# Optimization experiments

Hardware: AMD Instinct MI355X
Metric: run time of the kernel (lower is better)

Reference implementation:

```python
import jax, jax.numpy as jnp
import numpy as np

B, S, H = 64, 512, 768
A1, C1 = 100, 300          # token-attention and sentence-classifier hidden sizes
BETA = 1.0                 # soft_attention_beta
SLW, TLW, RLW = 1.0, 1.0, 0.01  # loss weights


def setup_inputs() -> dict:
    key = jax.random.key(0)
    ks = jax.random.split(key, 12)
    hidden_states = jax.random.normal(ks[0], (B, S, H), jnp.float32)
    # token_attention: Linear(H,100) -> Tanh -> Linear(100,1) -> Sigmoid
    w1 = jax.random.normal(ks[1], (H, A1), jnp.float32) * 0.02
    b1 = jnp.zeros((A1,), jnp.float32)
    w2 = jax.random.normal(ks[2], (A1, 1), jnp.float32) * 0.02
    b2 = jnp.zeros((1,), jnp.float32)
    # sentence_classification: Linear(H,300) -> Tanh -> Linear(300,1) -> Sigmoid
    sw1 = jax.random.normal(ks[3], (H, C1), jnp.float32) * 0.02
    sb1 = jnp.zeros((C1,), jnp.float32)
    sw2 = jax.random.normal(ks[4], (C1, 1), jnp.float32) * 0.02
    sb2 = jnp.zeros((1,), jnp.float32)
    offset_mapping = jax.random.randint(ks[5], (B, S, 2), 0, 4).astype(jnp.int32)
    offset_mapping = offset_mapping.at[:, 0, 0].set(0)  # first token starts a word
    # labels in {-1, 0, 1}; -1 = ignore
    labels = jax.random.randint(ks[6], (B, S), -1, 2).astype(jnp.float32)
    return {
        "hidden_states": hidden_states,
        "w1": w1, "b1": b1, "w2": w2, "b2": b2,
        "sw1": sw1, "sb1": sb1, "sw2": sw2, "sb2": sb2,
        "labels": labels,
        "offset_mapping": offset_mapping,
    }


def _forward(hidden_states, w1, b1, w2, b2, sw1, sb1, sw2, sb2, labels, offset_mapping):
    # token attention scores in (0,1): [B, S]
    token_att = jax.nn.sigmoid(
        jnp.tanh(hidden_states @ w1 + b1) @ w2 + b2
    )[..., 0]

    # ragged per-word subword max-pooling (segment-max along the sequence)
    not_subword = offset_mapping[:, :, 0] == 0                 # [B, S] word starts
    seg = jnp.maximum(jnp.cumsum(not_subword.astype(jnp.int32), axis=1) - 1, 0)

    def _seg_max(vals, seg_ids):
        return jax.ops.segment_max(vals, seg_ids, num_segments=S)

    segmax = jax.vmap(_seg_max)(token_att, seg)                # [B, S] per-word max
    word_att = jnp.where(not_subword, jnp.take_along_axis(segmax, seg, axis=1), 0.0)

    # mask: labeled tokens that are word starts
    token_mask = ((labels != -1) & not_subword).astype(token_att.dtype)
    masked = word_att * token_mask                              # token_logits [B, S]

    # beta-normalized soft attention pooling over hidden states
    p = masked ** BETA
    att_norm = p / jnp.sum(p, axis=1, keepdims=True)            # [B, S]
    pooled = jnp.einsum("bsh,bs->bh", hidden_states, att_norm)  # [B, H]

    sent = jax.nn.sigmoid(jnp.tanh(pooled @ sw1 + sb1) @ sw2 + sb2)  # [B, 1]

    # losses (MSE with reduction='sum')
    sentence_labels = jnp.max(labels, axis=1, keepdims=True)    # [B, 1]
    sentence_loss = jnp.sum((sent - sentence_labels) ** 2)
    zero_labels = jnp.where(labels != -1, labels, 0.0)
    token_loss = jnp.sum((masked - zero_labels) ** 2)
    ones_masked = jnp.where(masked == 0, 1.0, masked)
    reg_a = jnp.sum(jnp.min(ones_masked, axis=1, keepdims=True) ** 2)
    reg_b = jnp.sum((jnp.max(masked, axis=1, keepdims=True) - sentence_labels) ** 2)
    total = SLW * sentence_loss + TLW * token_loss + RLW * (reg_a + reg_b)
    return total, sentence_loss, token_loss, reg_a, reg_b, masked, sent


def reference(hidden_states, w1, b1, w2, b2, sw1, sb1, sw2, sb2, labels, offset_mapping):
    return _forward(hidden_states, w1, b1, w2, b2, sw1, sb1, sw2, sb2,
                    labels, offset_mapping)
```

## Files before the change

### kernel.cpp

```cpp
#include <hip/hip_runtime.h>
#include <math.h>

#define BB 64
#define SS 512
#define HH 768
#define AA1 100
#define CC1 300

typedef __bf16 bf16x8 __attribute__((ext_vector_type(8)));
typedef float f32x4 __attribute__((ext_vector_type(4)));

#ifndef __has_builtin
#define __has_builtin(x) 0
#endif
#if __has_builtin(__builtin_amdgcn_global_load_lds)
#define HAVE_GLL 1
#else
#define HAVE_GLL 0
#endif

#define AS1 __attribute__((address_space(1)))
#define AS3 __attribute__((address_space(3)))

__global__ __launch_bounds__(256) void k_prep(const float* __restrict__ w1,
                                              __bf16* __restrict__ w1i) {
    int idx = blockIdx.x * 256 + threadIdx.x;
    int j = idx % 112;
    int r = idx / 112;
    int e = r & 7, g = r >> 3;
    int k = (g >> 2) * 32 + (g & 3) * 8 + e;
    float v = (j < AA1) ? w1[k * AA1 + j] : 0.f;
    w1i[((size_t)g * 112 + j) * 8 + e] = (__bf16)v;
}

__global__ __launch_bounds__(256) void k_token_att(
        const float* __restrict__ hs, const __bf16* __restrict__ w1i,
        const float* __restrict__ b1, const float* __restrict__ w2,
        const float* __restrict__ b2, float* __restrict__ token_att) {
    __shared__ __attribute__((aligned(16))) float lA[4096];
    __shared__ __attribute__((aligned(16))) __bf16 lB[3584];

    const int tid = threadIdx.x;
    const int tok0 = blockIdx.x * 128;
    const int w = tid >> 6, lane = tid & 63;
    const int q = lane >> 4, ln = lane & 15;
    const int t0 = w * 32 + ln;
    const int t1 = t0 + 16;

    f32x4 acc0[7], acc1[7];
#pragma unroll
    for (int n = 0; n < 7; n++) {
        acc0[n] = (f32x4){0.f, 0.f, 0.f, 0.f};
        acc1[n] = (f32x4){0.f, 0.f, 0.f, 0.f};
    }

    const int p0 = (2 * q) ^ (ln & 7);
    const int p1 = (2 * q + 1) ^ (ln & 7);

    for (int kt = 0; kt < 24; kt++) {
        const int ko = kt * 32;
#pragma unroll
        for (int it = 0; it < 4; it++) {
            int i = tid + it * 256;
            int tt = i >> 3, c = (i & 7) ^ (tt & 7);
            const float* g = hs + (size_t)(tok0 + tt) * HH + ko + c * 4;
#if HAVE_GLL
            __builtin_amdgcn_global_load_lds((AS1 void*)g,
                    (AS3 void*)(lA + (it * 256 + w * 64) * 4), 16, 0, 0);
#else
            *(f32x4*)&lA[i * 4] = *(const f32x4*)g;
#endif
        }
        {
            const __bf16* gb0 = w1i + (size_t)kt * 3584 + (size_t)tid * 8;
#if HAVE_GLL
            __builtin_amdgcn_global_load_lds((AS1 void*)gb0,
                    (AS3 void*)(lB + (w * 64) * 8), 16, 0, 0);
            if (w < 3) {
                const __bf16* gb1 = w1i + (size_t)kt * 3584 + (size_t)(tid + 256) * 8;
                __builtin_amdgcn_global_load_lds((AS1 void*)gb1,
                        (AS3 void*)(lB + (256 + w * 64) * 8), 16, 0, 0);
            }
#else
            *(bf16x8*)&lB[(size_t)tid * 8] = *(const bf16x8*)gb0;
            if (tid < 192) {
                const __bf16* gb1 = w1i + (size_t)kt * 3584 + (size_t)(tid + 256) * 8;
                *(bf16x8*)&lB[(size_t)(tid + 256) * 8] = *(const bf16x8*)gb1;
            }
#endif
        }
        __syncthreads();
        f32x4 a00 = *(f32x4*)&lA[(t0 * 8 + p0) * 4];
        f32x4 a01 = *(f32x4*)&lA[(t0 * 8 + p1) * 4];
        f32x4 a10 = *(f32x4*)&lA[(t1 * 8 + p0) * 4];
        f32x4 a11 = *(f32x4*)&lA[(t1 * 8 + p1) * 4];
        bf16x8 af0, af1;
#pragma unroll
        for (int e = 0; e < 4; e++) {
            af0[e] = (__bf16)a00[e]; af0[e + 4] = (__bf16)a01[e];
            af1[e] = (__bf16)a10[e]; af1[e + 4] = (__bf16)a11[e];
        }
#pragma unroll
        for (int n = 0; n < 7; n++) {
            bf16x8 bf = *(bf16x8*)&lB[((size_t)q * 112 + n * 16 + ln) * 8];
            acc0[n] = __builtin_amdgcn_mfma_f32_16x16x32_bf16(af0, bf, acc0[n], 0, 0, 0);
            acc1[n] = __builtin_amdgcn_mfma_f32_16x16x32_bf16(af1, bf, acc1[n], 0, 0, 0);
        }
        __syncthreads();
    }

    float s0 = 0.f, s1 = 0.f, s2 = 0.f, s3 = 0.f;
    float u0 = 0.f, u1 = 0.f, u2 = 0.f, u3 = 0.f;
#pragma unroll
    for (int n = 0; n < 7; n++) {
        int j = n * 16 + ln;
        if (j < AA1) {
            float bj = b1[j], wj = w2[j];
            s0 += tanhf(acc0[n][0] + bj) * wj;
            s1 += tanhf(acc0[n][1] + bj) * wj;
            s2 += tanhf(acc0[n][2] + bj) * wj;
            s3 += tanhf(acc0[n][3] + bj) * wj;
            u0 += tanhf(acc1[n][0] + bj) * wj;
            u1 += tanhf(acc1[n][1] + bj) * wj;
            u2 += tanhf(acc1[n][2] + bj) * wj;
            u3 += tanhf(acc1[n][3] + bj) * wj;
        }
    }
#pragma unroll
    for (int off = 1; off < 16; off <<= 1) {
        s0 += __shfl_xor(s0, off); s1 += __shfl_xor(s1, off);
        s2 += __shfl_xor(s2, off); s3 += __shfl_xor(s3, off);
        u0 += __shfl_xor(u0, off); u1 += __shfl_xor(u1, off);
        u2 += __shfl_xor(u2, off); u3 += __shfl_xor(u3, off);
    }
    if (ln == 0) {
        float bb = b2[0];
        int base0 = tok0 + w * 32 + q * 4;
        int base1 = base0 + 16;
        token_att[base0 + 0] = 1.f / (1.f + expf(-(s0 + bb)));
        token_att[base0 + 1] = 1.f / (1.f + expf(-(s1 + bb)));
        token_att[base0 + 2] = 1.f / (1.f + expf(-(s2 + bb)));
        token_att[base0 + 3] = 1.f / (1.f + expf(-(s3 + bb)));
        token_att[base1 + 0] = 1.f / (1.f + expf(-(u0 + bb)));
        token_att[base1 + 1] = 1.f / (1.f + expf(-(u1 + bb)));
        token_att[base1 + 2] = 1.f / (1.f + expf(-(u2 + bb)));
        token_att[base1 + 3] = 1.f / (1.f + expf(-(u3 + bb)));
    }
}

__global__ __launch_bounds__(512) void k_mask(
        const float* __restrict__ token_att, const float* __restrict__ labels,
        const int* __restrict__ offm, float* __restrict__ masked_out,
        float* __restrict__ cw_g, short* __restrict__ cs_g,
        int* __restrict__ nnz_g, float* __restrict__ inv_g,
        float4* __restrict__ stats_g, float* __restrict__ out) {
    __shared__ int smax[512];
    __shared__ int wscan[8];
    __shared__ int wscan2[8];
    __shared__ float wred[5][8];

    const int b = blockIdx.x, s = threadIdx.x;
    const int lane = s & 63, wv = s >> 6;
    if (b == 0 && s < 5) out[s] = 0.f;
    const int ns = (offm[(b * SS + s) * 2] == 0) ? 1 : 0;

    int v = ns;
#pragma unroll
    for (int off = 1; off < 64; off <<= 1) {
        int o = __shfl_up(v, off);
        if (lane >= off) v += o;
    }
    if (lane == 63) wscan[wv] = v;
    smax[s] = 0;
    __syncthreads();
    int woff = 0;
    for (int i = 0; i < 8; i++) woff += (i < wv) ? wscan[i] : 0;
    const int seg = max(v + woff - 1, 0);

    const float ta = token_att[b * SS + s];
    atomicMax(&smax[seg], __float_as_int(ta));
    __syncthreads();

    const float wa = ns ? __int_as_float(smax[seg]) : 0.f;
    const float lab = labels[b * SS + s];
    const float m = (lab != -1.f && ns) ? wa : 0.f;
    masked_out[b * SS + s] = m;

    const float zl = (lab != -1.f) ? lab : 0.f;
    const float tl = (m - zl) * (m - zl);
    const float ones = (m == 0.f) ? 1.f : m;

    float r0 = m, r1 = tl, r2 = m, r3 = ones, r4 = lab;
#pragma unroll
    for (int off = 32; off > 0; off >>= 1) {
        r0 += __shfl_xor(r0, off);
        r1 += __shfl_xor(r1, off);
        r2 = fmaxf(r2, __shfl_xor(r2, off));
        r3 = fminf(r3, __shfl_xor(r3, off));
        r4 = fmaxf(r4, __shfl_xor(r4, off));
    }
    if (lane == 0) {
        wred[0][wv] = r0; wred[1][wv] = r1; wred[2][wv] = r2;
        wred[3][wv] = r3; wred[4][wv] = r4;
    }

    const int nz = (m != 0.f) ? 1 : 0;
    int v2 = nz;
#pragma unroll
    for (int off = 1; off < 64; off <<= 1) {
        int o = __shfl_up(v2, off);
        if (lane >= off) v2 += o;
    }
    if (lane == 63) wscan2[wv] = v2;
    __syncthreads();

    int woff2 = 0;
    for (int i = 0; i < 8; i++) woff2 += (i < wv) ? wscan2[i] : 0;
    if (nz) {
        int pos = v2 + woff2 - 1;
        cw_g[b * SS + pos] = m;
        cs_g[b * SS + pos] = (short)s;
    }
    if (s == 0) {
        float att = 0.f, tokl = 0.f, maxm = -1e30f, minone = 1e30f, slab = -1e30f;
        int nnz = 0;
        for (int i = 0; i < 8; i++) {
            att += wred[0][i]; tokl += wred[1][i];
            maxm = fmaxf(maxm, wred[2][i]);
            minone = fminf(minone, wred[3][i]);
            slab = fmaxf(slab, wred[4][i]);
            nnz += wscan2[i];
        }
        nnz_g[b] = nnz;
        inv_g[b] = 1.f / att;
        stats_g[b] = make_float4(tokl, maxm, minone, slab);
    }
}

__global__ __launch_bounds__(512) void k_poolsent(
        const float* __restrict__ hs, const float* __restrict__ cw_g,
        const short* __restrict__ cs_g, const int* __restrict__ nnz_g,
        const float* __restrict__ inv_g, const float4* __restrict__ stats_g,
        const float* __restrict__ sw1, const float* __restrict__ sb1,
        const float* __restrict__ sw2, const float* __restrict__ sb2,
        float* __restrict__ sent_out, float* __restrict__ out) {
    __shared__ float w[SS];
    __shared__ short idx[SS];
    __shared__ float pool[HH];
    __shared__ float wsum[8];

    const int b = blockIdx.x, tid = threadIdx.x;
    const int lane = tid & 63, wv = tid >> 6;
    const int nnz = nnz_g[b];
    if (tid < nnz) { w[tid] = cw_g[b * SS + tid]; idx[tid] = cs_g[b * SS + tid]; }
    __syncthreads();

    const float* hsb = hs + (size_t)b * SS * HH;
    const bool hi = (tid < 256);
    float a[8], c[8];
#pragma unroll
    for (int u = 0; u < 8; u++) { a[u] = 0.f; c[u] = 0.f; }
    int i = 0;
    for (; i + 8 <= nnz; i += 8) {
#pragma unroll
        for (int u = 0; u < 8; u++)
            a[u] += hsb[(size_t)idx[i + u] * HH + tid] * w[i + u];
        if (hi) {
#pragma unroll
            for (int u = 0; u < 8; u++)
                c[u] += hsb[(size_t)idx[i + u] * HH + 512 + tid] * w[i + u];
        }
    }
    for (; i < nnz; i++) {
        a[0] += hsb[(size_t)idx[i] * HH + tid] * w[i];
        if (hi) c[0] += hsb[(size_t)idx[i] * HH + 512 + tid] * w[i];
    }
    const float inv = inv_g[b];
    pool[tid] = (((a[0] + a[1]) + (a[2] + a[3])) + ((a[4] + a[5]) + (a[6] + a[7]))) * inv;
    if (hi)
        pool[512 + tid] = (((c[0] + c[1]) + (c[2] + c[3])) + ((c[4] + c[5]) + (c[6] + c[7]))) * inv;
    __syncthreads();

    float tt = 0.f;
    if (tid < CC1) {
        float z = sb1[tid];
#pragma unroll 8
        for (int k = 0; k < HH; k++) z += pool[k] * sw1[k * CC1 + tid];
        tt = tanhf(z) * sw2[tid];
    }
#pragma unroll
    for (int off = 32; off > 0; off >>= 1) tt += __shfl_xor(tt, off);
    if (lane == 0) wsum[wv] = tt;
    __syncthreads();
    if (tid == 0) {
        float zsum = wsum[0] + wsum[1] + wsum[2] + wsum[3] + wsum[4];
        float sv = 1.f / (1.f + expf(-(zsum + sb2[0])));
        sent_out[b] = sv;
        float4 st = stats_g[b];
        float vs = sv - st.w; vs *= vs;
        float ra = st.z * st.z;
        float rb = st.y - st.w; rb *= rb;
        atomicAdd(&out[1], vs);
        atomicAdd(&out[2], st.x);
        atomicAdd(&out[3], ra);
        atomicAdd(&out[4], rb);
        atomicAdd(&out[0], vs + st.x + 0.01f * (ra + rb));
    }
}

extern "C" void kernel_launch(void* const* d_in, const int* in_sizes, int n_in,
                              void* d_out, int out_size, void* d_ws, size_t ws_size,
                              hipStream_t stream) {
    const float* hs  = (const float*)d_in[0];
    const float* w1  = (const float*)d_in[1];
    const float* b1  = (const float*)d_in[2];
    const float* w2  = (const float*)d_in[3];
    const float* b2  = (const float*)d_in[4];
    const float* sw1 = (const float*)d_in[5];
    const float* sb1 = (const float*)d_in[6];
    const float* sw2 = (const float*)d_in[7];
    const float* sb2 = (const float*)d_in[8];
    const float* labels = (const float*)d_in[9];
    const int*   offm   = (const int*)d_in[10];

    float* out = (float*)d_out;
    float* ws  = (float*)d_ws;

    float*  token_att = ws;
    __bf16* w1i    = (__bf16*)(ws + 32768);
    float*  cw     = ws + 32768 + 43008;
    short*  cs     = (short*)(cw + 32768);
    int*    nnz    = (int*)(cw + 32768 + 16384);
    float*  inv    = (float*)(nnz + 64);
    float4* stats  = (float4*)(inv + 64);

    float* masked_out = out + 5;
    float* sent_out   = out + 5 + BB * SS;

    hipLaunchKernelGGL(k_prep, dim3(336), dim3(256), 0, stream, w1, w1i);
    hipLaunchKernelGGL(k_token_att, dim3(256), dim3(256), 0, stream,
                       hs, w1i, b1, w2, b2, token_att);
    hipLaunchKernelGGL(k_mask, dim3(BB), dim3(512), 0, stream,
                       token_att, labels, offm, masked_out,
                       cw, cs, nnz, inv, stats, out);
    hipLaunchKernelGGL(k_poolsent, dim3(BB), dim3(512), 0, stream,
                       hs, cw, cs, nnz, inv, stats,
                       sw1, sb1, sw2, sb2, sent_out, out);
}
```

Baseline: 247.4 us.

## Split pooling and sentence classifier into multi-block kernels with separate loss reduction

The single 64-block pool+classifier kernel is replaced by three kernels. k_pool uses a 64x12 grid to gather weighted hidden-state rows, splitting the nonzeros across four waves per 64-column chunk. k_sent uses a 64x5 grid that splits the 768x300 classifier matvec, with atomic accumulation into zsum. A single-wave k_losses then computes the sigmoid and reduces the losses with shuffles instead of global atomics. This spreads the latency-bound gather and matvec across many more CUs, at the cost of two extra launches and workspace reuse that overlaps earlier buffers.

```diff
diff --git a/kernel.cpp b/kernel.cpp
--- a/kernel.cpp
+++ b/kernel.cpp
@@ -153,7 +153,7 @@
         const int* __restrict__ offm, float* __restrict__ masked_out,
         float* __restrict__ cw_g, short* __restrict__ cs_g,
         int* __restrict__ nnz_g, float* __restrict__ inv_g,
-        float4* __restrict__ stats_g, float* __restrict__ out) {
+        float4* __restrict__ stats_g) {
     __shared__ int smax[512];
     __shared__ int wscan[8];
     __shared__ int wscan2[8];
@@ -161,7 +161,6 @@
 
     const int b = blockIdx.x, s = threadIdx.x;
     const int lane = s & 63, wv = s >> 6;
-    if (b == 0 && s < 5) out[s] = 0.f;
     const int ns = (offm[(b * SS + s) * 2] == 0) ? 1 : 0;
 
     int v = ns;
@@ -237,74 +236,107 @@
     }
 }
 
-__global__ __launch_bounds__(512) void k_poolsent(
+__global__ __launch_bounds__(256) void k_pool(
         const float* __restrict__ hs, const float* __restrict__ cw_g,
         const short* __restrict__ cs_g, const int* __restrict__ nnz_g,
-        const float* __restrict__ inv_g, const float4* __restrict__ stats_g,
-        const float* __restrict__ sw1, const float* __restrict__ sb1,
-        const float* __restrict__ sw2, const float* __restrict__ sb2,
-        float* __restrict__ sent_out, float* __restrict__ out) {
-    __shared__ float w[SS];
-    __shared__ short idx[SS];
-    __shared__ float pool[HH];
-    __shared__ float wsum[8];
-
-    const int b = blockIdx.x, tid = threadIdx.x;
-    const int lane = tid & 63, wv = tid >> 6;
+        const float* __restrict__ inv_g, float* __restrict__ pooled,
+        float* __restrict__ zsum) {
+    __shared__ float wl[SS];
+    __shared__ short il[SS];
+    __shared__ float red[256];
+
+    const int b = blockIdx.x, hc = blockIdx.y;
+    const int tid = threadIdx.x;
     const int nnz = nnz_g[b];
-    if (tid < nnz) { w[tid] = cw_g[b * SS + tid]; idx[tid] = cs_g[b * SS + tid]; }
-    __syncthreads();
-
-    const float* hsb = hs + (size_t)b * SS * HH;
-    const bool hi = (tid < 256);
-    float a[8], c[8];
-#pragma unroll
-    for (int u = 0; u < 8; u++) { a[u] = 0.f; c[u] = 0.f; }
-    int i = 0;
-    for (; i + 8 <= nnz; i += 8) {
-#pragma unroll
-        for (int u = 0; u < 8; u++)
-            a[u] += hsb[(size_t)idx[i + u] * HH + tid] * w[i + u];
-        if (hi) {
+    if (hc == 0 && tid == 0) zsum[b] = 0.f;
+    if (tid < nnz) { wl[tid] = cw_g[b * SS + tid]; il[tid] = cs_g[b * SS + tid]; }
+    if (tid + 256 < nnz) {
+        wl[tid + 256] = cw_g[b * SS + tid + 256];
+        il[tid + 256] = cs_g[b * SS + tid + 256];
+    }
+    __syncthreads();
+
+    const int h = (tid & 63) + hc * 64;
+    const int slot = tid >> 6;
+    const float* hsb = hs + (size_t)b * SS * HH + h;
+    const int len = (nnz + 3) >> 2;
+    const int i0 = slot * len;
+    const int i1 = min(i0 + len, nnz);
+    float a0 = 0.f, a1 = 0.f, a2 = 0.f, a3 = 0.f;
+    int i = i0;
+    for (; i + 4 <= i1; i += 4) {
+        a0 += hsb[(size_t)il[i]     * HH] * wl[i];
+        a1 += hsb[(size_t)il[i + 1] * HH] * wl[i + 1];
+        a2 += hsb[(size_t)il[i + 2] * HH] * wl[i + 2];
+        a3 += hsb[(size_t)il[i + 3] * HH] * wl[i + 3];
+    }
+    for (; i < i1; i++) a0 += hsb[(size_t)il[i] * HH] * wl[i];
+    red[tid] = (a0 + a1) + (a2 + a3);
+    __syncthreads();
+    if (tid < 64)
+        pooled[(size_t)b * HH + h] =
+            (red[tid] + red[tid + 64] + red[tid + 128] + red[tid + 192]) * inv_g[b];
+}
+
+__global__ __launch_bounds__(256) void k_sent(
+        const float* __restrict__ pooled, const float* __restrict__ sw1,
+        const float* __restrict__ sb1, const float* __restrict__ sw2,
+        float* __restrict__ zsum) {
+    __shared__ float pl[HH];
+    __shared__ float red[256];
+
+    const int b = blockIdx.x, cc = blockIdx.y;
+    const int tid = threadIdx.x;
+    pl[tid]       = pooled[(size_t)b * HH + tid];
+    pl[tid + 256] = pooled[(size_t)b * HH + tid + 256];
+    pl[tid + 512] = pooled[(size_t)b * HH + tid + 512];
+    __syncthreads();
+
+    const int cl = tid & 63, kq = tid >> 6;
+    const int c = cc * 60 + cl;
+    float z = 0.f;
+    if (cl < 60) {
+        const int k0 = kq * 192;
+        for (int k = k0; k < k0 + 192; k += 8) {
 #pragma unroll
             for (int u = 0; u < 8; u++)
-                c[u] += hsb[(size_t)idx[i + u] * HH + 512 + tid] * w[i + u];
-        }
-    }
-    for (; i < nnz; i++) {
-        a[0] += hsb[(size_t)idx[i] * HH + tid] * w[i];
-        if (hi) c[0] += hsb[(size_t)idx[i] * HH + 512 + tid] * w[i];
-    }
-    const float inv = inv_g[b];
-    pool[tid] = (((a[0] + a[1]) + (a[2] + a[3])) + ((a[4] + a[5]) + (a[6] + a[7]))) * inv;
-    if (hi)
-        pool[512 + tid] = (((c[0] + c[1]) + (c[2] + c[3])) + ((c[4] + c[5]) + (c[6] + c[7]))) * inv;
-    __syncthreads();
-
-    float tt = 0.f;
-    if (tid < CC1) {
-        float z = sb1[tid];
-#pragma unroll 8
-        for (int k = 0; k < HH; k++) z += pool[k] * sw1[k * CC1 + tid];
-        tt = tanhf(z) * sw2[tid];
-    }
-#pragma unroll
-    for (int off = 32; off > 0; off >>= 1) tt += __shfl_xor(tt, off);
-    if (lane == 0) wsum[wv] = tt;
-    __syncthreads();
-    if (tid == 0) {
-        float zsum = wsum[0] + wsum[1] + wsum[2] + wsum[3] + wsum[4];
-        float sv = 1.f / (1.f + expf(-(zsum + sb2[0])));
-        sent_out[b] = sv;
-        float4 st = stats_g[b];
-        float vs = sv - st.w; vs *= vs;
-        float ra = st.z * st.z;
-        float rb = st.y - st.w; rb *= rb;
-        atomicAdd(&out[1], vs);
-        atomicAdd(&out[2], st.x);
-        atomicAdd(&out[3], ra);
-        atomicAdd(&out[4], rb);
-        atomicAdd(&out[0], vs + st.x + 0.01f * (ra + rb));
+                z += pl[k + u] * sw1[(size_t)(k + u) * CC1 + c];
+        }
+    }
+    red[tid] = z;
+    __syncthreads();
+    if (kq == 0) {
+        float zz = red[tid] + red[tid + 64] + red[tid + 128] + red[tid + 192];
+        float t = 0.f;
+        if (cl < 60) t = tanhf(zz + sb1[c]) * sw2[c];
+#pragma unroll
+        for (int off = 32; off > 0; off >>= 1) t += __shfl_xor(t, off);
+        if (cl == 0) atomicAdd(&zsum[b], t);
+    }
+}
+
+__global__ __launch_bounds__(64) void k_losses(
+        const float* __restrict__ zsum, const float* __restrict__ sb2,
+        const float4* __restrict__ stats_g, float* __restrict__ sent_out,
+        float* __restrict__ out) {
+    const int b = threadIdx.x;
+    const float sv = 1.f / (1.f + expf(-(zsum[b] + sb2[0])));
+    sent_out[b] = sv;
+    const float4 st = stats_g[b];
+    float vs = sv - st.w; vs *= vs;
+    float ra = st.z * st.z;
+    float rb = st.y - st.w; rb *= rb;
+    float s0 = vs, s1 = st.x, s2 = ra, s3 = rb;
+#pragma unroll
+    for (int off = 32; off > 0; off >>= 1) {
+        s0 += __shfl_xor(s0, off);
+        s1 += __shfl_xor(s1, off);
+        s2 += __shfl_xor(s2, off);
+        s3 += __shfl_xor(s3, off);
+    }
+    if (b == 0) {
+        out[1] = s0; out[2] = s1; out[3] = s2; out[4] = s3;
+        out[0] = s0 + s1 + 0.01f * (s2 + s3);
     }
 }
 
@@ -333,6 +365,8 @@
     int*    nnz    = (int*)(cw + 32768 + 16384);
     float*  inv    = (float*)(nnz + 64);
     float4* stats  = (float4*)(inv + 64);
+    float*  pooled = ws;
+    float*  zsum   = ws + 49152;
 
     float* masked_out = out + 5;
     float* sent_out   = out + 5 + BB * SS;
@@ -342,8 +376,11 @@
                        hs, w1i, b1, w2, b2, token_att);
     hipLaunchKernelGGL(k_mask, dim3(BB), dim3(512), 0, stream,
                        token_att, labels, offm, masked_out,
-                       cw, cs, nnz, inv, stats, out);
-    hipLaunchKernelGGL(k_poolsent, dim3(BB), dim3(512), 0, stream,
-                       hs, cw, cs, nnz, inv, stats,
-                       sw1, sb1, sw2, sb2, sent_out, out);
-}
+                       cw, cs, nnz, inv, stats);
+    hipLaunchKernelGGL(k_pool, dim3(BB, 12), dim3(256), 0, stream,
+                       hs, cw, cs, nnz, inv, pooled, zsum);
+    hipLaunchKernelGGL(k_sent, dim3(BB, 5), dim3(256), 0, stream,
+                       pooled, sw1, sb1, sw2, zsum);
+    hipLaunchKernelGGL(k_losses, dim3(1), dim3(64), 0, stream,
+                       zsum, sb2, stats, sent_out, out);
+}
```

Measured after the change: 211.6 us. -14.5%, faster.
